# Kernel optimization log

Hardware: AMD Instinct MI355X
Metric: run time of the kernel (lower is better)

The kernel has to match this reference:

```python
import jax, jax.numpy as jnp
import numpy as np

TEMPERATURE = 0.5


def setup_inputs() -> dict:
    key = jax.random.key(0)
    k1, k2, k3, k4 = jax.random.split(key, 4)
    B, D = 4096, 256
    return {
        "emb_i": jax.random.normal(k1, (B, D), dtype=jnp.float32),
        "emb_j": jax.random.normal(k2, (B, D), dtype=jnp.float32),
        "tags": jax.random.randint(k3, (B,), 0, 100, dtype=jnp.int32),
        "num_classes": 100,
        "document_ids": jax.random.randint(k4, (B,), 0, 512, dtype=jnp.int32),
    }


def reference(emb_i, emb_j, tags, num_classes, document_ids):
    # L2-normalize rows (cosine similarity of normalized vectors == dot product)
    z_i = emb_i / jnp.linalg.norm(emb_i, axis=1, keepdims=True)
    z_j = emb_j / jnp.linalg.norm(emb_j, axis=1, keepdims=True)
    reps = jnp.concatenate([z_i, z_j], axis=0)          # [2B, D]
    sim = reps @ reps.T                                  # [2B, 2B]
    exp_sim = jnp.exp(sim / TEMPERATURE)                 # [2B, 2B]

    # sum(square(onehot_j - onehot_i))/2 == 1.0 iff labels differ, else 0.0
    tags2 = jnp.concatenate([tags, tags], axis=0)        # [2B]
    docs2 = jnp.concatenate([document_ids, document_ids], axis=0)
    mask = ((tags2[:, None] != tags2[None, :]) & (docs2[:, None] != docs2[None, :])).astype(exp_sim.dtype)

    denom = jnp.sum(mask * exp_sim, axis=1) + 0.1        # [2B]

    B = tags.shape[0]
    idx = jnp.arange(2 * B)
    pair = jnp.concatenate([jnp.arange(B) + B, jnp.arange(B)])  # partner index of each row
    numerator = exp_sim[idx, pair]                       # [2B]

    loss = jnp.sum(-jnp.log(numerator / denom)) / (2 * B)
    return loss
```

## Files before the change

### kernel.cpp

```cpp
#include <hip/hip_runtime.h>
#include <hip/hip_bf16.h>
#include <cstdint>
#include <cstddef>

#define B_ROWS 4096
#define D_DIM  256
#define TWOB   8192
static constexpr float kScale = 2.8853900817779268f;

typedef __bf16 bf16_t;
typedef __bf16 bf16x4 __attribute__((ext_vector_type(4)));
typedef __bf16 bf16x8 __attribute__((ext_vector_type(8)));
typedef float  f32x4  __attribute__((ext_vector_type(4)));

#define WS_Z    0ull
#define WS_KEYS ((size_t)TWOB * D_DIM * 2)
#define WS_DEN  (WS_KEYS + (size_t)TWOB * 4)
#define WS_PAIR (WS_DEN + (size_t)TWOB * 4)
#define WS_CNT  (WS_PAIR + (size_t)B_ROWS * 4)


__global__ __launch_bounds__(256) void prep_kernel(
    const float* __restrict__ emb_i, const float* __restrict__ emb_j,
    const int* __restrict__ tags, const int* __restrict__ docs,
    bf16_t* __restrict__ Z, int* __restrict__ keys,
    float* __restrict__ denom, float* __restrict__ pair, int* __restrict__ cnt)
{
  __shared__ float4 zbuf[4][64];
  const int t = threadIdx.x;
  const int lane = t & 63, w = t >> 6;
  const int b = blockIdx.x;
  const int rlocal = 2 * b + (w & 1);
  const int row = rlocal + (w >> 1) * B_ROWS;
  const float* src = (w >> 1) ? (emb_j + (size_t)rlocal * D_DIM)
                              : (emb_i + (size_t)rlocal * D_DIM);
  float4 v = *(const float4*)(src + lane * 4);
  float ss = v.x * v.x + v.y * v.y + v.z * v.z + v.w * v.w;
  #pragma unroll
  for (int m = 32; m; m >>= 1) ss += __shfl_xor(ss, m, 64);
  float inv = 1.0f / sqrtf(ss);
  float4 z = {v.x * inv, v.y * inv, v.z * inv, v.w * inv};
  zbuf[w][lane] = z;

  bf16x4 q;
  q[0] = (bf16_t)z.x; q[1] = (bf16_t)z.y; q[2] = (bf16_t)z.z; q[3] = (bf16_t)z.w;
  int chunk = lane >> 4;
  int g     = (lane >> 1) & 7;
  int gs    = g ^ (row & 7);
  int half  = lane & 1;
  *(bf16x4*)(Z + (size_t)row * D_DIM + chunk * 64 + gs * 8 + half * 4) = q;

  if (lane == 0) {
    keys[row] = (tags[rlocal] << 16) | docs[rlocal];
    denom[row] = 0.f;
  }
  if (b == 0 && t == 0) cnt[0] = 0;
  __syncthreads();
  if (w < 2) {
    float4 a = zbuf[w][lane], c = zbuf[w + 2][lane];
    float d = a.x * c.x + a.y * c.y + a.z * c.z + a.w * c.w;
    #pragma unroll
    for (int m = 32; m; m >>= 1) d += __shfl_xor(d, m, 64);
    if (lane == 0) pair[2 * b + w] = d;
  }
}

#define BM 128
#define BK 64
#define NKT (D_DIM / BK)
#define STRIP 4
#define TOT (STRIP * NKT)
#define NBLK 520

__global__ __launch_bounds__(256, 2) void fused_kernel(
    const bf16_t* __restrict__ Z, const int* __restrict__ keys,
    float* __restrict__ denom, const float* __restrict__ pair,
    int* __restrict__ cnt, float* __restrict__ out)
{
  __shared__ bf16_t sA[2][BM * BK];
  __shared__ bf16_t sB[2][BM * BK];
  __shared__ int s_last;
  __shared__ float s_red[4];
  const int tid  = threadIdx.x;
  const int lane = tid & 63;
  const int w    = tid >> 6;
  const int wr = w >> 1, wc = w & 1;
  const int l15 = lane & 15, l4 = lane >> 4;

  const int bid = (blockIdx.x % 8) * (NBLK / 8) + blockIdx.x / 8;

  int t0 = 4 * bid;
  int rt = (int)((sqrtf(8.0f * (float)t0 + 1.0f) - 1.0f) * 0.5f);
  while ((rt + 1) * (rt + 2) / 2 <= t0) ++rt;
  while (rt * (rt + 1) / 2 > t0) --rt;
  int ct = t0 - rt * (rt + 1) / 2;
  int r0s[STRIP], c0s[STRIP];
  bool od[STRIP];
  #pragma unroll
  for (int i = 0; i < STRIP; ++i) {
    r0s[i] = rt * BM; c0s[i] = ct * BM; od[i] = (rt != ct);
    if (++ct > rt) { ++rt; ct = 0; }
  }

  f32x4 acc[4][4];
  const f32x4 vzero = {0.f, 0.f, 0.f, 0.f};
  #pragma unroll
  for (int mi = 0; mi < 4; ++mi)
    #pragma unroll
    for (int ni = 0; ni < 4; ++ni) acc[mi][ni] = vzero;

  auto STAGE = [&](int buf, int ti, int kt) {
    #pragma unroll
    for (int i = 0; i < 4; ++i) {
      int o  = i * 4096 + tid * 16;
      int rl = o >> 7, ob = o & 127;
      const bf16_t* ga = Z + (size_t)(r0s[ti] + rl) * D_DIM + kt * 64 + (ob >> 1);
      __builtin_amdgcn_global_load_lds(
          (const __attribute__((address_space(1))) void*)ga,
          (__attribute__((address_space(3))) void*)((char*)&sA[buf][0] + o), 16, 0, 0);
      const bf16_t* gb = Z + (size_t)(c0s[ti] + rl) * D_DIM + kt * 64 + (ob >> 1);
      __builtin_amdgcn_global_load_lds(
          (const __attribute__((address_space(1))) void*)gb,
          (__attribute__((address_space(3))) void*)((char*)&sB[buf][0] + o), 16, 0, 0);
    }
  };

  auto EPI = [&](int ti) {
    const int row0 = r0s[ti], col0 = c0s[ti];
    int keyr[4][4];
    #pragma unroll
    for (int mi = 0; mi < 4; ++mi)
      #pragma unroll
      for (int j = 0; j < 4; ++j)
        keyr[mi][j] = keys[row0 + wr * 64 + mi * 16 + l4 * 4 + j];
    int keyc[4];
    #pragma unroll
    for (int ni = 0; ni < 4; ++ni)
      keyc[ni] = keys[col0 + wc * 64 + ni * 16 + l15];

    float rowsum[4][4];
    #pragma unroll
    for (int mi = 0; mi < 4; ++mi)
      #pragma unroll
      for (int j = 0; j < 4; ++j) rowsum[mi][j] = 0.f;
    float colsum[4] = {0.f, 0.f, 0.f, 0.f};

    #pragma unroll
    for (int ni = 0; ni < 4; ++ni) {
      #pragma unroll
      for (int mi = 0; mi < 4; ++mi) {
        #pragma unroll
        for (int j = 0; j < 4; ++j) {
          int x = keyr[mi][j] ^ keyc[ni];
          bool m = ((x >> 16) != 0) & ((x & 0xFFFF) != 0);
          float e = m ? __builtin_amdgcn_exp2f(acc[mi][ni][j] * kScale) : 0.f;
          rowsum[mi][j] += e;
          colsum[ni] += e;
        }
      }
    }
    #pragma unroll
    for (int mi = 0; mi < 4; ++mi)
      #pragma unroll
      for (int j = 0; j < 4; ++j) {
        float v = rowsum[mi][j];
        v += __shfl_xor(v, 1, 64);
        v += __shfl_xor(v, 2, 64);
        v += __shfl_xor(v, 4, 64);
        v += __shfl_xor(v, 8, 64);
        if (l15 == 0)
          atomicAdd(&denom[row0 + wr * 64 + mi * 16 + l4 * 4 + j], v);
      }
    if (od[ti]) {
      #pragma unroll
      for (int ni = 0; ni < 4; ++ni) {
        float v = colsum[ni];
        v += __shfl_xor(v, 16, 64);
        v += __shfl_xor(v, 32, 64);
        if (l4 == 0)
          atomicAdd(&denom[col0 + wc * 64 + ni * 16 + l15], v);
      }
    }
    #pragma unroll
    for (int mi = 0; mi < 4; ++mi)
      #pragma unroll
      for (int ni = 0; ni < 4; ++ni) acc[mi][ni] = vzero;
  };

  STAGE(0, 0, 0);
  #pragma unroll
  for (int s = 0; s < TOT; ++s) {
    const int buf = s & 1;
    __builtin_amdgcn_s_barrier();
    if (s + 1 < TOT) {
      STAGE(buf ^ 1, (s + 1) >> 2, (s + 1) & 3);
      asm volatile("s_waitcnt vmcnt(8)" ::: "memory");
    } else {
      asm volatile("s_waitcnt vmcnt(0)" ::: "memory");
    }
    __builtin_amdgcn_s_barrier();
    __builtin_amdgcn_sched_barrier(0);

    bf16x8 af[2][4], bfr[2][4];
    #pragma unroll
    for (int h = 0; h < 2; ++h) {
      #pragma unroll
      for (int mi = 0; mi < 4; ++mi) {
        int rl  = wr * 64 + mi * 16 + l15;
        int gsa = (h * 4 + l4) ^ (rl & 7);
        af[h][mi] = *(const bf16x8*)(&sA[buf][rl * 64 + gsa * 8]);
        int cl  = wc * 64 + mi * 16 + l15;
        int gsb = (h * 4 + l4) ^ (cl & 7);
        bfr[h][mi] = *(const bf16x8*)(&sB[buf][cl * 64 + gsb * 8]);
      }
    }
    #pragma unroll
    for (int h = 0; h < 2; ++h)
      #pragma unroll
      for (int mi = 0; mi < 4; ++mi)
        #pragma unroll
        for (int ni = 0; ni < 4; ++ni)
          acc[mi][ni] = __builtin_amdgcn_mfma_f32_16x16x32_bf16(
              af[h][mi], bfr[h][ni], acc[mi][ni], 0, 0, 0);

    if ((s & 3) == 3) EPI(s >> 2);
  }

  __syncthreads();
  if (tid == 0) {
    int done = __hip_atomic_fetch_add(cnt, 1, __ATOMIC_ACQ_REL, __HIP_MEMORY_SCOPE_AGENT);
    s_last = (done == NBLK - 1) ? 1 : 0;
  }
  __syncthreads();
  if (s_last) {
    float c = 0.f;
    #pragma unroll
    for (int i = 0; i < 32; ++i) {
      float d = __hip_atomic_load(&denom[i * 256 + tid], __ATOMIC_RELAXED,
                                  __HIP_MEMORY_SCOPE_AGENT);
      c += __logf(d + 0.1f);
    }
    #pragma unroll
    for (int i = 0; i < 16; ++i) c -= 4.0f * pair[i * 256 + tid];
    #pragma unroll
    for (int m = 32; m; m >>= 1) c += __shfl_xor(c, m, 64);
    if (lane == 0) s_red[w] = c;
    __syncthreads();
    if (tid == 0)
      out[0] = (s_red[0] + s_red[1] + s_red[2] + s_red[3]) * (1.0f / (float)TWOB);
  }
}

extern "C" void kernel_launch(void* const* d_in, const int* in_sizes, int n_in,
                              void* d_out, int out_size, void* d_ws, size_t ws_size,
                              hipStream_t stream) {
  const float* emb_i = (const float*)d_in[0];
  const float* emb_j = (const float*)d_in[1];
  const int*   tags  = (const int*)d_in[2];
  const int*   docs  = (const int*)d_in[4];

  char* ws = (char*)d_ws;
  bf16_t* Z     = (bf16_t*)(ws + WS_Z);
  int*    keys  = (int*)(ws + WS_KEYS);
  float*  denom = (float*)(ws + WS_DEN);
  float*  pair  = (float*)(ws + WS_PAIR);
  int*    cnt   = (int*)(ws + WS_CNT);
  float*  out   = (float*)d_out;

  prep_kernel<<<B_ROWS / 2, 256, 0, stream>>>(emb_i, emb_j, tags, docs, Z, keys, denom, pair, cnt);
  fused_kernel<<<NBLK, 256, 0, stream>>>(Z, keys, denom, pair, cnt, out);
}
```

Baseline: 144.0 us.

## Enlarge GEMM tiles to 256x256 with 512-thread blocks over the lower triangle

Raises the tile size from 128x128 to 256x256, uses 8 waves per block with 128x64 per-wave subtiles, and launches 256 blocks that each handle two or three triangular tiles, with tiles strided by NBLK instead of taken as contiguous strips. Larger tiles halve global/LDS traffic per FLOP and cut the number of atomic denominator updates. In exchange LDS use doubles to 128KB per block, accumulator registers double, the pipeline now uses full __syncthreads with no explicit vmcnt tuning, and blocks get uneven amounts of work (2 vs 3 tiles).

New measurement: 132.5 us. -8.0%, faster.

```diff
diff --git a/kernel.cpp b/kernel.cpp
--- a/kernel.cpp
+++ b/kernel.cpp
@@ -65,14 +65,13 @@
   }
 }
 
-#define BM 128
-#define BK 64
-#define NKT (D_DIM / BK)
-#define STRIP 4
-#define TOT (STRIP * NKT)
-#define NBLK 520
-
-__global__ __launch_bounds__(256, 2) void fused_kernel(
+#define BM   256
+#define BK   64
+#define NRT  (TWOB / BM)
+#define NTIL (NRT * (NRT + 1) / 2)
+#define NBLK 256
+
+__global__ __launch_bounds__(512, 2) void fused_kernel(
     const bf16_t* __restrict__ Z, const int* __restrict__ keys,
     float* __restrict__ denom, const float* __restrict__ pair,
     int* __restrict__ cnt, float* __restrict__ out)
@@ -80,98 +79,113 @@
   __shared__ bf16_t sA[2][BM * BK];
   __shared__ bf16_t sB[2][BM * BK];
   __shared__ int s_last;
-  __shared__ float s_red[4];
+  __shared__ float s_red[8];
   const int tid  = threadIdx.x;
   const int lane = tid & 63;
   const int w    = tid >> 6;
-  const int wr = w >> 1, wc = w & 1;
+  const int wr = w >> 2, wc = w & 3;
   const int l15 = lane & 15, l4 = lane >> 4;
 
-  const int bid = (blockIdx.x % 8) * (NBLK / 8) + blockIdx.x / 8;
-
-  int t0 = 4 * bid;
-  int rt = (int)((sqrtf(8.0f * (float)t0 + 1.0f) - 1.0f) * 0.5f);
-  while ((rt + 1) * (rt + 2) / 2 <= t0) ++rt;
-  while (rt * (rt + 1) / 2 > t0) --rt;
-  int ct = t0 - rt * (rt + 1) / 2;
-  int r0s[STRIP], c0s[STRIP];
-  bool od[STRIP];
-  #pragma unroll
-  for (int i = 0; i < STRIP; ++i) {
-    r0s[i] = rt * BM; c0s[i] = ct * BM; od[i] = (rt != ct);
-    if (++ct > rt) { ++rt; ct = 0; }
-  }
-
-  f32x4 acc[4][4];
+  const int bid = (blockIdx.x & 7) * (NBLK / 8) + (blockIdx.x >> 3);
+
+  auto decode = [](int t, int& rt, int& ct) {
+    int r = (int)((sqrtf(8.0f * (float)t + 1.0f) - 1.0f) * 0.5f);
+    while ((r + 1) * (r + 2) / 2 <= t) ++r;
+    while (r * (r + 1) / 2 > t) --r;
+    rt = r; ct = t - r * (r + 1) / 2;
+  };
+  const bool has3 = (bid < NTIL - 2 * NBLK);
+  int rt, ct;
+  decode(bid, rt, ct);
+  const int r0a = rt * BM, c0a = ct * BM; const bool oda = (rt != ct);
+  decode(bid + NBLK, rt, ct);
+  const int r0b = rt * BM, c0b = ct * BM; const bool odb = (rt != ct);
+  int r0c = 0, c0c = 0; bool odc = false;
+  if (has3) { decode(bid + 2 * NBLK, rt, ct); r0c = rt * BM; c0c = ct * BM; odc = (rt != ct); }
+
+  f32x4 acc[8][4];
   const f32x4 vzero = {0.f, 0.f, 0.f, 0.f};
   #pragma unroll
-  for (int mi = 0; mi < 4; ++mi)
+  for (int mi = 0; mi < 8; ++mi)
     #pragma unroll
     for (int ni = 0; ni < 4; ++ni) acc[mi][ni] = vzero;
 
-  auto STAGE = [&](int buf, int ti, int kt) {
+  auto STAGE = [&](int buf, int row0, int col0, int kt) {
     #pragma unroll
     for (int i = 0; i < 4; ++i) {
-      int o  = i * 4096 + tid * 16;
+      int o  = i * 8192 + tid * 16;
       int rl = o >> 7, ob = o & 127;
-      const bf16_t* ga = Z + (size_t)(r0s[ti] + rl) * D_DIM + kt * 64 + (ob >> 1);
+      const bf16_t* ga = Z + (size_t)(row0 + rl) * D_DIM + kt * 64 + (ob >> 1);
       __builtin_amdgcn_global_load_lds(
           (const __attribute__((address_space(1))) void*)ga,
           (__attribute__((address_space(3))) void*)((char*)&sA[buf][0] + o), 16, 0, 0);
-      const bf16_t* gb = Z + (size_t)(c0s[ti] + rl) * D_DIM + kt * 64 + (ob >> 1);
+      const bf16_t* gb = Z + (size_t)(col0 + rl) * D_DIM + kt * 64 + (ob >> 1);
       __builtin_amdgcn_global_load_lds(
           (const __attribute__((address_space(1))) void*)gb,
           (__attribute__((address_space(3))) void*)((char*)&sB[buf][0] + o), 16, 0, 0);
     }
   };
 
-  auto EPI = [&](int ti) {
-    const int row0 = r0s[ti], col0 = c0s[ti];
-    int keyr[4][4];
-    #pragma unroll
-    for (int mi = 0; mi < 4; ++mi)
-      #pragma unroll
-      for (int j = 0; j < 4; ++j)
-        keyr[mi][j] = keys[row0 + wr * 64 + mi * 16 + l4 * 4 + j];
+  auto COMPUTE = [&](int buf) {
+    #pragma unroll
+    for (int h = 0; h < 2; ++h) {
+      bf16x8 bfr[4];
+      #pragma unroll
+      for (int ni = 0; ni < 4; ++ni) {
+        int cl  = wc * 64 + ni * 16 + l15;
+        int gsb = (h * 4 + l4) ^ (cl & 7);
+        bfr[ni] = *(const bf16x8*)(&sB[buf][cl * 64 + gsb * 8]);
+      }
+      #pragma unroll
+      for (int mi = 0; mi < 8; ++mi) {
+        int rl  = wr * 128 + mi * 16 + l15;
+        int gsa = (h * 4 + l4) ^ (rl & 7);
+        bf16x8 af = *(const bf16x8*)(&sA[buf][rl * 64 + gsa * 8]);
+        #pragma unroll
+        for (int ni = 0; ni < 4; ++ni)
+          acc[mi][ni] = __builtin_amdgcn_mfma_f32_16x16x32_bf16(
+              af, bfr[ni], acc[mi][ni], 0, 0, 0);
+      }
+    }
+  };
+
+  auto EPI = [&](int row0, int col0, bool od) {
     int keyc[4];
     #pragma unroll
     for (int ni = 0; ni < 4; ++ni)
       keyc[ni] = keys[col0 + wc * 64 + ni * 16 + l15];
-
-    float rowsum[4][4];
-    #pragma unroll
-    for (int mi = 0; mi < 4; ++mi)
-      #pragma unroll
-      for (int j = 0; j < 4; ++j) rowsum[mi][j] = 0.f;
     float colsum[4] = {0.f, 0.f, 0.f, 0.f};
-
-    #pragma unroll
-    for (int ni = 0; ni < 4; ++ni) {
-      #pragma unroll
-      for (int mi = 0; mi < 4; ++mi) {
+    #pragma unroll
+    for (int mi = 0; mi < 8; ++mi) {
+      int keyr[4];
+      #pragma unroll
+      for (int j = 0; j < 4; ++j)
+        keyr[j] = keys[row0 + wr * 128 + mi * 16 + l4 * 4 + j];
+      float rowsum[4] = {0.f, 0.f, 0.f, 0.f};
+      #pragma unroll
+      for (int ni = 0; ni < 4; ++ni) {
         #pragma unroll
         for (int j = 0; j < 4; ++j) {
-          int x = keyr[mi][j] ^ keyc[ni];
+          int x = keyr[j] ^ keyc[ni];
           bool m = ((x >> 16) != 0) & ((x & 0xFFFF) != 0);
           float e = m ? __builtin_amdgcn_exp2f(acc[mi][ni][j] * kScale) : 0.f;
-          rowsum[mi][j] += e;
+          rowsum[j] += e;
           colsum[ni] += e;
         }
-      }
-    }
-    #pragma unroll
-    for (int mi = 0; mi < 4; ++mi)
+        acc[mi][ni] = vzero;
+      }
       #pragma unroll
       for (int j = 0; j < 4; ++j) {
-        float v = rowsum[mi][j];
+        float v = rowsum[j];
         v += __shfl_xor(v, 1, 64);
         v += __shfl_xor(v, 2, 64);
         v += __shfl_xor(v, 4, 64);
         v += __shfl_xor(v, 8, 64);
         if (l15 == 0)
-          atomicAdd(&denom[row0 + wr * 64 + mi * 16 + l4 * 4 + j], v);
-      }
-    if (od[ti]) {
+          atomicAdd(&denom[row0 + wr * 128 + mi * 16 + l4 * 4 + j], v);
+      }
+    }
+    if (od) {
       #pragma unroll
       for (int ni = 0; ni < 4; ++ni) {
         float v = colsum[ni];
@@ -181,50 +195,24 @@
           atomicAdd(&denom[col0 + wc * 64 + ni * 16 + l15], v);
       }
     }
-    #pragma unroll
-    for (int mi = 0; mi < 4; ++mi)
-      #pragma unroll
-      for (int ni = 0; ni < 4; ++ni) acc[mi][ni] = vzero;
-  };
-
-  STAGE(0, 0, 0);
-  #pragma unroll
-  for (int s = 0; s < TOT; ++s) {
-    const int buf = s & 1;
-    __builtin_amdgcn_s_barrier();
-    if (s + 1 < TOT) {
-      STAGE(buf ^ 1, (s + 1) >> 2, (s + 1) & 3);
-      asm volatile("s_waitcnt vmcnt(8)" ::: "memory");
-    } else {
-      asm volatile("s_waitcnt vmcnt(0)" ::: "memory");
-    }
-    __builtin_amdgcn_s_barrier();
-    __builtin_amdgcn_sched_barrier(0);
-
-    bf16x8 af[2][4], bfr[2][4];
-    #pragma unroll
-    for (int h = 0; h < 2; ++h) {
-      #pragma unroll
-      for (int mi = 0; mi < 4; ++mi) {
-        int rl  = wr * 64 + mi * 16 + l15;
-        int gsa = (h * 4 + l4) ^ (rl & 7);
-        af[h][mi] = *(const bf16x8*)(&sA[buf][rl * 64 + gsa * 8]);
-        int cl  = wc * 64 + mi * 16 + l15;
-        int gsb = (h * 4 + l4) ^ (cl & 7);
-        bfr[h][mi] = *(const bf16x8*)(&sB[buf][cl * 64 + gsb * 8]);
-      }
-    }
-    #pragma unroll
-    for (int h = 0; h < 2; ++h)
-      #pragma unroll
-      for (int mi = 0; mi < 4; ++mi)
-        #pragma unroll
-        for (int ni = 0; ni < 4; ++ni)
-          acc[mi][ni] = __builtin_amdgcn_mfma_f32_16x16x32_bf16(
-              af[h][mi], bfr[h][ni], acc[mi][ni], 0, 0, 0);
-
-    if ((s & 3) == 3) EPI(s >> 2);
-  }
+  };
+
+  auto TILE = [&](int row0, int col0, bool od, bool don, int nr, int nc) {
+    #pragma unroll
+    for (int kt = 0; kt < 4; ++kt) {
+      const int buf = kt & 1;
+      __syncthreads();
+      if (kt < 3)      STAGE(buf ^ 1, row0, col0, kt + 1);
+      else if (don)    STAGE(buf ^ 1, nr, nc, 0);
+      COMPUTE(buf);
+      if (kt == 3) EPI(row0, col0, od);
+    }
+  };
+
+  STAGE(0, r0a, c0a, 0);
+  TILE(r0a, c0a, oda, true, r0b, c0b);
+  TILE(r0b, c0b, odb, has3, r0c, c0c);
+  if (has3) TILE(r0c, c0c, odc, false, 0, 0);
 
   __syncthreads();
   if (tid == 0) {
@@ -235,19 +223,23 @@
   if (s_last) {
     float c = 0.f;
     #pragma unroll
-    for (int i = 0; i < 32; ++i) {
-      float d = __hip_atomic_load(&denom[i * 256 + tid], __ATOMIC_RELAXED,
+    for (int i = 0; i < 16; ++i) {
+      float d = __hip_atomic_load(&denom[i * 512 + tid], __ATOMIC_RELAXED,
                                   __HIP_MEMORY_SCOPE_AGENT);
       c += __logf(d + 0.1f);
     }
     #pragma unroll
-    for (int i = 0; i < 16; ++i) c -= 4.0f * pair[i * 256 + tid];
+    for (int i = 0; i < 8; ++i) c -= 4.0f * pair[i * 512 + tid];
     #pragma unroll
     for (int m = 32; m; m >>= 1) c += __shfl_xor(c, m, 64);
     if (lane == 0) s_red[w] = c;
     __syncthreads();
-    if (tid == 0)
-      out[0] = (s_red[0] + s_red[1] + s_red[2] + s_red[3]) * (1.0f / (float)TWOB);
+    if (tid == 0) {
+      float s = 0.f;
+      #pragma unroll
+      for (int i = 0; i < 8; ++i) s += s_red[i];
+      out[0] = s * (1.0f / (float)TWOB);
+    }
   }
 }
 
@@ -268,5 +260,5 @@
   float*  out   = (float*)d_out;
 
   prep_kernel<<<B_ROWS / 2, 256, 0, stream>>>(emb_i, emb_j, tags, docs, Z, keys, denom, pair, cnt);
-  fused_kernel<<<NBLK, 256, 0, stream>>>(Z, keys, denom, pair, cnt, out);
+  fused_kernel<<<NBLK, 512, 0, stream>>>(Z, keys, denom, pair, cnt, out);
 }
```
